# Optimization experiments

Hardware: AMD Instinct MI355X
Metric: run time of the kernel (lower is better)

The kernel has to match this reference:

```python
import jax, jax.numpy as jnp
import numpy as np

N = 8192
E = 131072
IN = 512
H = 8
C = 128
HC = H * C
EPS = 1e-5
NEG_SLOPE = 0.2


def _gatv2(x, src, dst, Wl, bl, Wr, br, att, bias):
    """GATv2Conv (PyG semantics, concat=True, self-loops already in src/dst)."""
    n = x.shape[0]
    xl = (x @ Wl + bl).reshape(n, H, C)  # source transform (lin_l)
    xr = (x @ Wr + br).reshape(n, H, C)  # dest transform (lin_r)
    m = xl[src] + xr[dst]                # [E,H,C] per-edge message
    e = jnp.einsum('ehc,hc->eh', jax.nn.leaky_relu(m, NEG_SLOPE), att)  # [E,H]
    # segment softmax over destination nodes
    emax = jax.ops.segment_max(e, dst, num_segments=n)
    w = jnp.exp(e - emax[dst])
    denom = jax.ops.segment_sum(w, dst, num_segments=n)
    alpha = w / denom[dst]               # [E,H]
    out = jax.ops.segment_sum(alpha[:, :, None] * xl[src], dst, num_segments=n)
    return out.reshape(n, HC) + bias


def _bn(x, gamma, beta):
    mu = jnp.mean(x, axis=0)
    var = jnp.mean((x - mu) ** 2, axis=0)
    return (x - mu) * jax.lax.rsqrt(var + EPS) * gamma + beta


def setup_inputs() -> dict:
    key = jax.random.key(0)
    ks = jax.random.split(key, 16)
    s = 0.05
    return {
        'x': jax.random.normal(ks[0], (N, IN), jnp.float32),
        'edge_index': jax.random.randint(ks[1], (2, E), 0, N, jnp.int32),
        'W1l': jax.random.normal(ks[2], (IN, HC), jnp.float32) * s,
        'b1l': jnp.zeros((HC,), jnp.float32),
        'W1r': jax.random.normal(ks[3], (IN, HC), jnp.float32) * s,
        'b1r': jnp.zeros((HC,), jnp.float32),
        'att1': jax.random.normal(ks[4], (H, C), jnp.float32) * s,
        'bias1': jnp.zeros((HC,), jnp.float32),
        'g1': jnp.ones((HC,), jnp.float32),
        'beta1': jnp.zeros((HC,), jnp.float32),
        'W2l': jax.random.normal(ks[5], (HC, HC), jnp.float32) * s,
        'b2l': jnp.zeros((HC,), jnp.float32),
        'W2r': jax.random.normal(ks[6], (HC, HC), jnp.float32) * s,
        'b2r': jnp.zeros((HC,), jnp.float32),
        'att2': jax.random.normal(ks[7], (H, C), jnp.float32) * s,
        'bias2': jnp.zeros((HC,), jnp.float32),
        'g2': jnp.ones((HC,), jnp.float32),
        'beta2': jnp.zeros((HC,), jnp.float32),
    }


def reference(x, edge_index, W1l, b1l, W1r, b1r, att1, bias1, g1, beta1,
              W2l, b2l, W2r, b2r, att2, bias2, g2, beta2):
    n = x.shape[0]
    loops = jnp.arange(n, dtype=edge_index.dtype)
    src = jnp.concatenate([edge_index[0], loops])
    dst = jnp.concatenate([edge_index[1], loops])
    h = _gatv2(x, src, dst, W1l, b1l, W1r, b1r, att1, bias1)
    h = jax.nn.elu(_bn(h, g1, beta1))
    h = _gatv2(h, src, dst, W2l, b2l, W2r, b2r, att2, bias2)
    h = jax.nn.elu(_bn(h, g2, beta2))
    return h
```

## Files before the change

### kernel.cpp

```cpp
#include <hip/hip_runtime.h>
#include <stdint.h>

#define NN     8192
#define NEDGE  131072
#define NETOT  (NEDGE + NN)
#define K_IN   512
#define HC_    1024
#define NOUT   2048
#define BNEPS  1e-5f
#define SLOPE  0.2f

typedef __bf16 bf16x8 __attribute__((ext_vector_type(8)));
typedef float  f32x4  __attribute__((ext_vector_type(4)));
typedef float  f32x2  __attribute__((ext_vector_type(2)));

__device__ __forceinline__ float bf2f(unsigned short u) {
  union { uint32_t u; float f; } c; c.u = ((uint32_t)u) << 16; return c.f;
}
__device__ __forceinline__ unsigned short f2bf(float f) {
  union { float f; uint32_t u; } c; c.f = f;
  uint32_t r = c.u + 0x7fffu + ((c.u >> 16) & 1u);
  return (unsigned short)(r >> 16);
}
__device__ __forceinline__ f32x2 upk2(uint32_t u) {
  union { uint32_t u; float f; } a, b;
  a.u = u << 16; b.u = u & 0xffff0000u;
  f32x2 r; r.x = a.f; r.y = b.f; return r;
}

__device__ __forceinline__ void gload16(const void* g, void* l) {
  __builtin_amdgcn_global_load_lds(
      (const __attribute__((address_space(1))) uint32_t*)g,
      (__attribute__((address_space(3))) uint32_t*)l, 16, 0, 0);
}

#define SBAR() do { asm volatile("" ::: "memory"); __builtin_amdgcn_s_barrier(); asm volatile("" ::: "memory"); } while (0)
#define VMC(n) asm volatile("s_waitcnt vmcnt(" #n ")" ::: "memory")

__global__ __launch_bounds__(256) void k_cvt_bf16(const float* __restrict__ in,
                                                  unsigned short* __restrict__ out, int n4) {
  int i = blockIdx.x * 256 + threadIdx.x;
  if (i >= n4) return;
  float4 v = *(const float4*)&in[(size_t)i * 4];
  ushort4 o;
  o.x = f2bf(v.x); o.y = f2bf(v.y); o.z = f2bf(v.z); o.w = f2bf(v.w);
  *(ushort4*)&out[(size_t)i * 4] = o;
}

__global__ __launch_bounds__(256) void k_transpose2_bf16(const float* __restrict__ Wa,
                                                         const float* __restrict__ Wb,
                                                         unsigned short* __restrict__ Wt,
                                                         int K, int N) {
  __shared__ float tile[32][33];
  const float* W = blockIdx.z ? Wb : Wa;
  unsigned short* dst = Wt + (size_t)blockIdx.z * N * K;
  int n0 = blockIdx.x * 32, k0 = blockIdx.y * 32;
  int tx = threadIdx.x & 31, ty = threadIdx.x >> 5;
  for (int i = ty; i < 32; i += 8)
    tile[i][tx] = W[(size_t)(k0 + i) * N + n0 + tx];
  __syncthreads();
  for (int i = ty; i < 32; i += 8)
    dst[(size_t)(n0 + i) * K + k0 + tx] = f2bf(tile[tx][i]);
}

__global__ __launch_bounds__(256) void k_hist(const int* __restrict__ ei, int* __restrict__ cnt) {
  int i = blockIdx.x * 256 + threadIdx.x;
  if (i >= NETOT) return;
  int d = (i < NEDGE) ? ei[NEDGE + i] : (i - NEDGE);
  atomicAdd(&cnt[d], 1);
}

__global__ __launch_bounds__(256) void k_scan(const int* __restrict__ cnt,
                                              int* __restrict__ rowptr,
                                              int* __restrict__ cursor) {
  __shared__ int part[256];
  int t = threadIdx.x;
  int base = t * 32;
  int s = 0;
  for (int i = 0; i < 32; ++i) s += cnt[base + i];
  part[t] = s;
  __syncthreads();
  for (int off = 1; off < 256; off <<= 1) {
    int u = (t >= off) ? part[t - off] : 0;
    __syncthreads();
    part[t] += u;
    __syncthreads();
  }
  int run = part[t] - s;
  for (int i = 0; i < 32; ++i) {
    rowptr[base + i] = run;
    cursor[base + i] = run;
    run += cnt[base + i];
  }
  if (t == 255) rowptr[NN] = run;
}

__global__ __launch_bounds__(256) void k_scatter(const int* __restrict__ ei,
                                                 int* __restrict__ cursor,
                                                 int* __restrict__ srcs) {
  int i = blockIdx.x * 256 + threadIdx.x;
  if (i >= NETOT) return;
  int s, d;
  if (i < NEDGE) { s = ei[i]; d = ei[NEDGE + i]; }
  else           { s = d = i - NEDGE; }
  int pos = atomicAdd(&cursor[d], 1);
  srcs[pos] = s;
}

__global__ __launch_bounds__(512, 2) void k_gemm256(const unsigned short* __restrict__ A,
                                                    const unsigned short* __restrict__ Bt,
                                                    const float* __restrict__ biasL,
                                                    const float* __restrict__ biasR,
                                                    unsigned short* __restrict__ C,
                                                    int K) {
  __shared__ unsigned short lA[2][256 * 64];
  __shared__ unsigned short lB[2][256 * 64];

  const int bid = blockIdx.x;
  const int xcd = bid & 7, idx = bid >> 3;
  const int m0 = (xcd * 4 + (idx & 3)) * 256;
  const int n0 = (idx >> 2) * 256;

  const int tid = threadIdx.x;
  const int l   = tid & 63;
  const int wv  = tid >> 6;
  const int wm  = wv >> 2, wn = wv & 3;
  const int l15 = l & 15, l4 = l >> 4;

  const int srow = tid >> 3;
  const int ssgk = (tid & 7) ^ (srow & 7);

  const f32x4 vzero = {0.f, 0.f, 0.f, 0.f};
  f32x4 acc[8][4];
#pragma unroll
  for (int i = 0; i < 8; ++i)
#pragma unroll
    for (int j = 0; j < 4; ++j) acc[i][j] = vzero;

  bf16x8 a2[8];
  bf16x8 bb[2][4];

  auto stageA = [&](int kt, int h) {
    const int buf = kt & 1;
    const size_t go = (size_t)(m0 + h * 128 + srow) * K + (size_t)kt * 64 + ssgk * 8;
    unsigned short* lp = &lA[buf][h * 8192 + tid * 8];
    gload16(&A[go], lp);
    gload16(&A[go + (size_t)64 * K], lp + 4096);
  };
  auto stageB = [&](int kt, int h) {
    const int buf = kt & 1;
    const size_t go = (size_t)(n0 + h * 128 + srow) * K + (size_t)kt * 64 + ssgk * 8;
    unsigned short* lp = &lB[buf][h * 8192 + tid * 8];
    gload16(&Bt[go], lp);
    gload16(&Bt[go + (size_t)64 * K], lp + 4096);
  };
  auto readA = [&](int buf, int qm) {
#pragma unroll
    for (int fm = 0; fm < 4; ++fm)
#pragma unroll
      for (int kk = 0; kk < 2; ++kk) {
        int r = qm * 128 + wm * 64 + fm * 16 + l15;
        int g = (kk * 4 + l4) ^ (r & 7);
        a2[fm * 2 + kk] = *(const bf16x8*)&lA[buf][r * 64 + g * 8];
      }
  };
  auto readB = [&](int buf, int qn) {
#pragma unroll
    for (int fn = 0; fn < 2; ++fn)
#pragma unroll
      for (int kk = 0; kk < 2; ++kk) {
        int r = qn * 128 + wn * 32 + fn * 16 + l15;
        int g = (kk * 4 + l4) ^ (r & 7);
        bb[qn][fn * 2 + kk] = *(const bf16x8*)&lB[buf][r * 64 + g * 8];
      }
  };
  auto quad = [&](int qm, int qn) {
    __builtin_amdgcn_s_setprio(1);
#pragma unroll
    for (int fm = 0; fm < 4; ++fm)
#pragma unroll
      for (int fn = 0; fn < 2; ++fn)
#pragma unroll
        for (int kk = 0; kk < 2; ++kk)
          acc[qm * 4 + fm][qn * 2 + fn] = __builtin_amdgcn_mfma_f32_16x16x32_bf16(
              a2[fm * 2 + kk], bb[qn][fn * 2 + kk], acc[qm * 4 + fm][qn * 2 + fn], 0, 0, 0);
    __builtin_amdgcn_s_setprio(0);
  };

  const int NT = K >> 6;

  stageA(0, 0); stageB(0, 0); stageB(0, 1); stageA(0, 1);

  for (int t = 0; t < NT - 1; ++t) {
    const int buf = t & 1;
    stageA(t + 1, 0);
    VMC(6); SBAR();
    readA(buf, 0); readB(buf, 0);
    quad(0, 0);
    stageB(t + 1, 0);
    VMC(6); SBAR();
    readB(buf, 1);
    quad(0, 1);
    stageB(t + 1, 1);
    VMC(6); SBAR();
    readA(buf, 1);
    quad(1, 0);
    stageA(t + 1, 1);
    quad(1, 1);
  }
  {
    const int buf = (NT - 1) & 1;
    VMC(4); SBAR();
    readA(buf, 0); readB(buf, 0);
    quad(0, 0);
    VMC(2); SBAR();
    readB(buf, 1);
    quad(0, 1);
    VMC(0); SBAR();
    readA(buf, 1);
    quad(1, 0);
    quad(1, 1);
  }

  const float* bias = (n0 < HC_) ? biasL : (biasR - HC_);
#pragma unroll
  for (int fm = 0; fm < 8; ++fm) {
    int row0 = m0 + (fm >> 2) * 128 + wm * 64 + (fm & 3) * 16 + l4 * 4;
#pragma unroll
    for (int fn = 0; fn < 4; ++fn) {
      int col = n0 + (fn >> 1) * 128 + wn * 32 + (fn & 1) * 16 + l15;
      float bv = bias[col];
#pragma unroll
      for (int j = 0; j < 4; ++j)
        C[(size_t)(row0 + j) * NOUT + col] = f2bf(acc[fm][fn][j] + bv);
    }
  }
}

template <bool OUT_BF16>
__global__ __launch_bounds__(256, 7) void k_edge_agg(const unsigned short* __restrict__ XLR,
                                                     const float* __restrict__ att,
                                                     const float* __restrict__ bias,
                                                     const int* __restrict__ rowptr,
                                                     const int* __restrict__ srcs,
                                                     void* __restrict__ outp) {
  const int tid  = threadIdx.x;
  const int wv   = tid >> 6;
  const int d    = blockIdx.x * 2 + (wv >> 1);
  const int half = wv & 1;
  const int l    = tid & 63;
  const int c0   = half * 512 + l * 8;

  f32x2 attv[4], xrv[4];
  {
    const f32x2* ap = (const f32x2*)&att[c0];
    attv[0] = ap[0]; attv[1] = ap[1]; attv[2] = ap[2]; attv[3] = ap[3];
    uint4 u = *(const uint4*)&XLR[(size_t)d * NOUT + HC_ + c0];
    xrv[0] = upk2(u.x); xrv[1] = upk2(u.y); xrv[2] = upk2(u.z); xrv[3] = upk2(u.w);
  }

  f32x2 acc0 = {0.f, 0.f}, acc1 = {0.f, 0.f}, acc2 = {0.f, 0.f}, acc3 = {0.f, 0.f};
  float den = 0.f;

  const int beg = __builtin_amdgcn_readfirstlane(rowptr[d]);
  const int end = __builtin_amdgcn_readfirstlane(rowptr[d + 1]);
  const int e1  = end - 1;

  auto rowp = [&](int s) { return (const uint4*)&XLR[(size_t)s * NOUT + c0]; };
  auto cl   = [&](int i) { return i < e1 ? i : e1; };

  uint4 R0 = *rowp(srcs[beg]);
  uint4 R1 = *rowp(srcs[cl(beg + 1)]);
  uint4 R2 = *rowp(srcs[cl(beg + 2)]);
  uint4 R3 = *rowp(srcs[cl(beg + 3)]);
  int sN1 = srcs[cl(beg + 4)];
  int sN2 = srcs[cl(beg + 5)];
  int sN3 = srcs[cl(beg + 6)];

  int i = beg;

#define STEP(R)                                                                \
  {                                                                            \
    f32x2 x0 = upk2(R.x), x1 = upk2(R.y), x2 = upk2(R.z), x3 = upk2(R.w);      \
    R = *rowp(sN1);                                                            \
    sN1 = sN2; sN2 = sN3;                                                      \
    sN3 = srcs[cl(i + 7)];                                                     \
    f32x2 ps = {0.f, 0.f}, y;                                                  \
    y = x0 + xrv[0]; ps = __builtin_elementwise_max(y, y * SLOPE) * attv[0] + ps; \
    y = x1 + xrv[1]; ps = __builtin_elementwise_max(y, y * SLOPE) * attv[1] + ps; \
    y = x2 + xrv[2]; ps = __builtin_elementwise_max(y, y * SLOPE) * attv[2] + ps; \
    y = x3 + xrv[3]; ps = __builtin_elementwise_max(y, y * SLOPE) * attv[3] + ps; \
    float p = ps.x + ps.y;                                                     \
    p += __shfl_xor(p, 1);                                                     \
    p += __shfl_xor(p, 2);                                                     \
    p += __shfl_xor(p, 4);                                                     \
    p += __shfl_xor(p, 8);                                                     \
    float wgt = __expf(p);                                                     \
    den += wgt;                                                                \
    f32x2 w2 = {wgt, wgt};                                                     \
    acc0 = w2 * x0 + acc0;                                                     \
    acc1 = w2 * x1 + acc1;                                                     \
    acc2 = w2 * x2 + acc2;                                                     \
    acc3 = w2 * x3 + acc3;                                                     \
    ++i;                                                                       \
  }

  while (true) {
    STEP(R0); if (i == end) break;
    STEP(R1); if (i == end) break;
    STEP(R2); if (i == end) break;
    STEP(R3); if (i == end) break;
  }
#undef STEP

  const float inv = 1.0f / den;
  const f32x2* bp = (const f32x2*)&bias[c0];
  float o[8];
  o[0] = acc0.x * inv + bp[0].x; o[1] = acc0.y * inv + bp[0].y;
  o[2] = acc1.x * inv + bp[1].x; o[3] = acc1.y * inv + bp[1].y;
  o[4] = acc2.x * inv + bp[2].x; o[5] = acc2.y * inv + bp[2].y;
  o[6] = acc3.x * inv + bp[3].x; o[7] = acc3.y * inv + bp[3].y;

  if (OUT_BF16) {
    unsigned short* op = (unsigned short*)outp + (size_t)d * HC_ + c0;
    ushort4 u0, u1;
    u0.x = f2bf(o[0]); u0.y = f2bf(o[1]); u0.z = f2bf(o[2]); u0.w = f2bf(o[3]);
    u1.x = f2bf(o[4]); u1.y = f2bf(o[5]); u1.z = f2bf(o[6]); u1.w = f2bf(o[7]);
    *(ushort4*)&op[0] = u0;
    *(ushort4*)&op[4] = u1;
  } else {
    float* op = (float*)outp + (size_t)d * HC_ + c0;
    float4 v0 = {o[0], o[1], o[2], o[3]};
    float4 v1 = {o[4], o[5], o[6], o[7]};
    *(float4*)&op[0] = v0;
    *(float4*)&op[4] = v1;
  }
}

__global__ __launch_bounds__(256) void k_colstats4(const unsigned short* __restrict__ X,
                                                   float* __restrict__ stats) {
  int col = threadIdx.x * 4;
  int r0 = blockIdx.y * 128;
  f32x2 s01 = {0.f, 0.f}, s23 = {0.f, 0.f}, q01 = {0.f, 0.f}, q23 = {0.f, 0.f};
  for (int r = r0; r < r0 + 128; ++r) {
    uint2 v = *(const uint2*)&X[(size_t)r * HC_ + col];
    f32x2 a = upk2(v.x), b = upk2(v.y);
    s01 = s01 + a; s23 = s23 + b;
    q01 = a * a + q01; q23 = b * b + q23;
  }
  atomicAdd(&stats[col + 0], s01.x);
  atomicAdd(&stats[col + 1], s01.y);
  atomicAdd(&stats[col + 2], s23.x);
  atomicAdd(&stats[col + 3], s23.y);
  atomicAdd(&stats[HC_ + col + 0], q01.x);
  atomicAdd(&stats[HC_ + col + 1], q01.y);
  atomicAdd(&stats[HC_ + col + 2], q23.x);
  atomicAdd(&stats[HC_ + col + 3], q23.y);
}

template <bool OUT_BF16>
__global__ __launch_bounds__(256) void k_bn_elu(const unsigned short* __restrict__ Xp,
                                                const float* __restrict__ stats,
                                                const float* __restrict__ gamma,
                                                const float* __restrict__ beta,
                                                void* __restrict__ outp) {
  size_t idx = (size_t)blockIdx.x * 256 + threadIdx.x;
  size_t e0 = idx * 4;
  int col = (int)(e0 & (HC_ - 1));
  float xs[4];
  ushort4 u = *(const ushort4*)&Xp[e0];
  xs[0] = bf2f(u.x); xs[1] = bf2f(u.y); xs[2] = bf2f(u.z); xs[3] = bf2f(u.w);
  float os[4];
  const float rn = 1.0f / (float)NN;
#pragma unroll
  for (int j = 0; j < 4; ++j) {
    int c = col + j;
    float mu = stats[c] * rn;
    float var = stats[HC_ + c] * rn - mu * mu;
    float v = (xs[j] - mu) * rsqrtf(var + BNEPS) * gamma[c] + beta[c];
    os[j] = v > 0.f ? v : (__expf(v) - 1.f);
  }
  if (OUT_BF16) {
    ushort4 o;
    o.x = f2bf(os[0]); o.y = f2bf(os[1]); o.z = f2bf(os[2]); o.w = f2bf(os[3]);
    *(ushort4*)&((unsigned short*)outp)[e0] = o;
  } else {
    float4 o = {os[0], os[1], os[2], os[3]};
    *(float4*)&((float*)outp)[e0] = o;
  }
}

extern "C" void kernel_launch(void* const* d_in, const int* in_sizes, int n_in,
                              void* d_out, int out_size, void* d_ws, size_t ws_size,
                              hipStream_t stream) {
  const float* x     = (const float*)d_in[0];
  const int*   ei    = (const int*)d_in[1];
  const float* W1l   = (const float*)d_in[2];
  const float* b1l   = (const float*)d_in[3];
  const float* W1r   = (const float*)d_in[4];
  const float* b1r   = (const float*)d_in[5];
  const float* att1  = (const float*)d_in[6];
  const float* bias1 = (const float*)d_in[7];
  const float* g1    = (const float*)d_in[8];
  const float* be1   = (const float*)d_in[9];
  const float* W2l   = (const float*)d_in[10];
  const float* b2l   = (const float*)d_in[11];
  const float* W2r   = (const float*)d_in[12];
  const float* b2r   = (const float*)d_in[13];
  const float* att2  = (const float*)d_in[14];
  const float* bias2 = (const float*)d_in[15];
  const float* g2    = (const float*)d_in[16];
  const float* be2   = (const float*)d_in[17];
  float* out = (float*)d_out;

  char* wsb = (char*)d_ws;
  size_t o = 0;
  auto alloc = [&](size_t b) {
    void* p = wsb + o;
    o = (o + b + 255) & ~(size_t)255;
    return p;
  };
  unsigned short* xbf  = (unsigned short*)alloc((size_t)NN * K_IN * 2);
  unsigned short* wT1  = (unsigned short*)alloc((size_t)NOUT * K_IN * 2);
  unsigned short* wT2  = (unsigned short*)alloc((size_t)NOUT * HC_ * 2);
  unsigned short* XLR  = (unsigned short*)alloc((size_t)NN * NOUT * 2);
  unsigned short* h0   = (unsigned short*)alloc((size_t)NN * HC_ * 2);
  int* cnt     = (int*)alloc((size_t)NN * 4);
  int* rowptr  = (int*)alloc((size_t)(NN + 1) * 4);
  int* cursor  = (int*)alloc((size_t)NN * 4);
  int* srcs    = (int*)alloc((size_t)NETOT * 4);
  float* stats = (float*)alloc((size_t)2 * HC_ * 4);

  hipMemsetAsync(cnt, 0, (size_t)NN * 4, stream);
  hipMemsetAsync(stats, 0, (size_t)2 * HC_ * 4, stream);

  k_cvt_bf16<<<(NN * K_IN / 4 + 255) / 256, 256, 0, stream>>>(x, xbf, NN * K_IN / 4);
  k_transpose2_bf16<<<dim3(HC_ / 32, K_IN / 32, 2), 256, 0, stream>>>(W1l, W1r, wT1, K_IN, HC_);
  k_transpose2_bf16<<<dim3(HC_ / 32, HC_ / 32, 2), 256, 0, stream>>>(W2l, W2r, wT2, HC_, HC_);

  k_hist<<<(NETOT + 255) / 256, 256, 0, stream>>>(ei, cnt);
  k_scan<<<1, 256, 0, stream>>>(cnt, rowptr, cursor);
  k_scatter<<<(NETOT + 255) / 256, 256, 0, stream>>>(ei, cursor, srcs);

  k_gemm256<<<256, 512, 0, stream>>>(xbf, wT1, b1l, b1r, XLR, K_IN);
  k_edge_agg<true><<<NN / 2, 256, 0, stream>>>(XLR, att1, bias1, rowptr, srcs, h0);
  k_colstats4<<<dim3(1, NN / 128), 256, 0, stream>>>(h0, stats);
  k_bn_elu<true><<<NN * HC_ / 4 / 256, 256, 0, stream>>>(h0, stats, g1, be1, h0);

  k_gemm256<<<256, 512, 0, stream>>>(h0, wT2, b2l, b2r, XLR, HC_);
  k_edge_agg<true><<<NN / 2, 256, 0, stream>>>(XLR, att2, bias2, rowptr, srcs, h0);
  hipMemsetAsync(stats, 0, (size_t)2 * HC_ * 4, stream);
  k_colstats4<<<dim3(1, NN / 128), 256, 0, stream>>>(h0, stats);
  k_bn_elu<false><<<NN * HC_ / 4 / 256, 256, 0, stream>>>(h0, stats, g2, be2, out);
}
```

Before: 243.2 us.

## Restructure GEMM main loop into two-tile-ahead prefetch with explicit LDS waits

```diff
diff --git a/kernel.cpp b/kernel.cpp
--- a/kernel.cpp
+++ b/kernel.cpp
@@ -36,6 +36,7 @@
 
 #define SBAR() do { asm volatile("" ::: "memory"); __builtin_amdgcn_s_barrier(); asm volatile("" ::: "memory"); } while (0)
 #define VMC(n) asm volatile("s_waitcnt vmcnt(" #n ")" ::: "memory")
+#define LGKM0() do { asm volatile("s_waitcnt lgkmcnt(0)" ::: "memory"); __builtin_amdgcn_sched_barrier(0); } while (0)
 
 __global__ __launch_bounds__(256) void k_cvt_bf16(const float* __restrict__ in,
                                                   unsigned short* __restrict__ out, int n4) {
@@ -140,15 +141,13 @@
   bf16x8 a2[8];
   bf16x8 bb[2][4];
 
-  auto stageA = [&](int kt, int h) {
-    const int buf = kt & 1;
+  auto stageA = [&](int kt, int h, int buf) {
     const size_t go = (size_t)(m0 + h * 128 + srow) * K + (size_t)kt * 64 + ssgk * 8;
     unsigned short* lp = &lA[buf][h * 8192 + tid * 8];
     gload16(&A[go], lp);
     gload16(&A[go + (size_t)64 * K], lp + 4096);
   };
-  auto stageB = [&](int kt, int h) {
-    const int buf = kt & 1;
+  auto stageB = [&](int kt, int h, int buf) {
     const size_t go = (size_t)(n0 + h * 128 + srow) * K + (size_t)kt * 64 + ssgk * 8;
     unsigned short* lp = &lB[buf][h * 8192 + tid * 8];
     gload16(&Bt[go], lp);
@@ -188,39 +187,66 @@
   };
 
   const int NT = K >> 6;
-
-  stageA(0, 0); stageB(0, 0); stageB(0, 1); stageA(0, 1);
-
-  for (int t = 0; t < NT - 1; ++t) {
-    const int buf = t & 1;
-    stageA(t + 1, 0);
-    VMC(6); SBAR();
-    readA(buf, 0); readB(buf, 0);
-    quad(0, 0);
-    stageB(t + 1, 0);
-    VMC(6); SBAR();
-    readB(buf, 1);
-    quad(0, 1);
-    stageB(t + 1, 1);
-    VMC(6); SBAR();
-    readA(buf, 1);
-    quad(1, 0);
-    stageA(t + 1, 1);
-    quad(1, 1);
-  }
-  {
-    const int buf = (NT - 1) & 1;
-    VMC(4); SBAR();
-    readA(buf, 0); readB(buf, 0);
-    quad(0, 0);
-    VMC(2); SBAR();
-    readB(buf, 1);
-    quad(0, 1);
-    VMC(0); SBAR();
-    readA(buf, 1);
-    quad(1, 0);
-    quad(1, 1);
-  }
+  const int NI = NT / 2 - 1;
+
+  stageA(0, 0, 0); stageB(0, 0, 0); stageB(0, 1, 0); stageA(0, 1, 0);
+  stageA(1, 0, 1); stageB(1, 0, 1); stageB(1, 1, 1); stageA(1, 1, 1);
+  VMC(12);
+  SBAR();
+
+  for (int i = 0; i < NI; ++i) {
+    const int t2 = 2 * i + 2, t3 = 2 * i + 3;
+    readA(0, 0); readB(0, 0);
+    VMC(10); SBAR(); LGKM0();
+    quad(0, 0); SBAR();
+    readB(0, 1);
+    stageA(t2, 0, 0); stageB(t2, 0, 0);
+    VMC(12); SBAR(); LGKM0();
+    quad(0, 1); SBAR();
+    readA(0, 1);
+    stageB(t2, 1, 0);
+    SBAR(); LGKM0();
+    quad(1, 0); SBAR();
+    stageA(t2, 1, 0);
+    VMC(12); SBAR();
+    quad(1, 1); SBAR();
+    readA(1, 0); readB(1, 0);
+    VMC(10); SBAR(); LGKM0();
+    quad(0, 0); SBAR();
+    readB(1, 1);
+    stageA(t3, 0, 1); stageB(t3, 0, 1);
+    VMC(12); SBAR(); LGKM0();
+    quad(0, 1); SBAR();
+    readA(1, 1);
+    stageB(t3, 1, 1);
+    SBAR(); LGKM0();
+    quad(1, 0); SBAR();
+    stageA(t3, 1, 1);
+    VMC(12); SBAR();
+    quad(1, 1); SBAR();
+  }
+
+  readA(0, 0); readB(0, 0);
+  VMC(10); SBAR(); LGKM0();
+  quad(0, 0); SBAR();
+  readB(0, 1);
+  VMC(8); SBAR(); LGKM0();
+  quad(0, 1); SBAR();
+  readA(0, 1);
+  SBAR(); LGKM0();
+  quad(1, 0); SBAR();
+  VMC(4); SBAR();
+  quad(1, 1); SBAR();
+  readA(1, 0); readB(1, 0);
+  VMC(2); SBAR(); LGKM0();
+  quad(0, 0); SBAR();
+  readB(1, 1);
+  VMC(0); SBAR(); LGKM0();
+  quad(0, 1); SBAR();
+  readA(1, 1);
+  SBAR(); LGKM0();
+  quad(1, 0); SBAR();
+  quad(1, 1);
 
   const float* bias = (n0 < HC_) ? biasL : (biasR - HC_);
 #pragma unroll
```

Result: no change. 245.2 us (+0.8%).
